# Optimization experiments

Hardware: AMD Instinct MI355X
Metric: run time of the kernel (lower is better)

Reference implementation:

```python
import jax, jax.numpy as jnp
import numpy as np

N, D, E, L = 50000, 64, 800000, 2


def _normalize(x):
    n = jnp.linalg.norm(x, axis=-1, keepdims=True)
    return x / jnp.maximum(n, 1e-12)


def _mobius_add(x, y, c):
    xy = jnp.sum(x * y, -1, keepdims=True)
    x2 = jnp.sum(x * x, -1, keepdims=True)
    y2 = jnp.sum(y * y, -1, keepdims=True)
    num = (1 + 2 * c * xy + c * y2) * x + (1 - c * x2) * y
    den = 1 + 2 * c * xy + (c ** 2) * x2 * y2
    return num / den


def _log_map(x, y, c):
    d = _mobius_add(-x, y, c)
    dn = jnp.maximum(jnp.linalg.norm(d, axis=-1, keepdims=True), 1e-10)
    return 2.0 / jnp.sqrt(c) * jnp.arctanh(jnp.sqrt(c) * dn) * d / dn


def _exp_map(x, v, c):
    vn = jnp.maximum(jnp.linalg.norm(v, axis=-1, keepdims=True), 1e-10)
    second = jnp.tanh(jnp.sqrt(c) * vn / 2.0) * v / (jnp.sqrt(c) * vn)
    return _mobius_add(x, second, c)


def _mean_agg(h, src, dst, n):
    # copy_u('h') then mean over incoming edges; empty neighborhoods -> 0 (DGL semantics)
    s = jax.ops.segment_sum(h[src], dst, num_segments=n)
    cnt = jax.ops.segment_sum(jnp.ones((src.shape[0],), h.dtype), dst, num_segments=n)
    return s / jnp.maximum(cnt, 1.0)[:, None]


def setup_inputs() -> dict:
    key = jax.random.key(0)
    ks = jax.random.split(key, 12)
    scale = 1.0 / np.sqrt(D)
    e_emb = jax.random.normal(ks[0], (N, D), jnp.float32)
    b_emb = jax.random.normal(ks[1], (N, D), jnp.float32) * (0.3 * scale)  # inside Poincare ball
    s_emb = jax.random.normal(ks[2], (N, D), jnp.float32)
    src = jax.random.randint(ks[3], (E,), 0, N, jnp.int32)
    dst = jax.random.randint(ks[4], (E,), 0, N, jnp.int32)
    We = jax.random.normal(ks[5], (L, D, D), jnp.float32) * scale
    Wb = jax.random.normal(ks[6], (L, D, D), jnp.float32) * scale
    Ws = jax.random.normal(ks[7], (L, D, D), jnp.float32) * scale
    be = jnp.zeros((L, D), jnp.float32)
    bb = jnp.zeros((L, D), jnp.float32)
    bs = jnp.zeros((L, D), jnp.float32)
    b_curvature = jnp.ones((1,), jnp.float32)
    s_curvature = jnp.ones((1,), jnp.float32)
    return {"e_emb": e_emb, "b_emb": b_emb, "s_emb": s_emb,
            "We": We, "be": be, "Wb": Wb, "bb": bb, "Ws": Ws, "bs": bs,
            "b_curvature": b_curvature, "s_curvature": s_curvature,
            "src": src, "dst": dst}


def reference(e_emb, b_emb, s_emb, We, be, Wb, bb, Ws, bs, b_curvature, s_curvature, src, dst):
    n = e_emb.shape[0]
    bc = b_curvature[0]
    sc = s_curvature[0]  # spherical path does not use curvature in the original forward math
    zero = jnp.zeros_like(b_emb)
    for l in range(We.shape[0]):
        # euclidean: linear -> mean aggregate -> LeakyReLU(0.2)
        h = e_emb @ We[l].T + be[l]
        e_emb = jax.nn.leaky_relu(_mean_agg(h, src, dst, n), 0.2)
        # hyperbolic: log map at origin -> linear -> mean aggregate -> exp map at origin
        tan = _log_map(zero, b_emb, bc)
        hb = tan @ Wb[l].T + bb[l]
        b_emb = _exp_map(zero, _mean_agg(hb, src, dst, n), bc)
        # spherical: normalize -> linear -> normalize -> mean aggregate -> normalize
        hs = _normalize(_normalize(s_emb) @ Ws[l].T + bs[l])
        s_emb = _normalize(_mean_agg(hs, src, dst, n))
    return (e_emb, b_emb, s_emb)
```

## Files before the change

kernel.cpp:

```cpp
#include <hip/hip_runtime.h>
#include <hip/hip_bf16.h>

#define DIM 64

typedef __attribute__((ext_vector_type(4)))  float f32x4;
typedef __attribute__((ext_vector_type(2)))  float f32x2;
typedef __attribute__((ext_vector_type(8)))  short short8;
typedef __attribute__((ext_vector_type(4)))  unsigned short u16x4;
typedef __attribute__((ext_vector_type(2)))  unsigned int u32x2;

static __device__ __forceinline__ float wave_sum64(float v) {
    v += __shfl_xor(v, 1, 64);
    v += __shfl_xor(v, 2, 64);
    v += __shfl_xor(v, 4, 64);
    v += __shfl_xor(v, 8, 64);
    v += __shfl_xor(v, 16, 64);
    v += __shfl_xor(v, 32, 64);
    return v;
}

static __device__ __forceinline__ float b2f(unsigned short u) {
    return __uint_as_float(((unsigned int)u) << 16);
}
static __device__ __forceinline__ unsigned short f2b(float f) {
    unsigned int u = __float_as_uint(f);
    unsigned int rounded = u + 0x7fff + ((u >> 16) & 1);
    return (unsigned short)(rounded >> 16);
}
static __device__ __forceinline__ float b2f_lo(unsigned int u) {
    return __uint_as_float(u << 16);
}
static __device__ __forceinline__ float b2f_hi(unsigned int u) {
    return __uint_as_float(u & 0xffff0000u);
}

#define PCHUNK 8192
#define BCAP 4096

__global__ __launch_bounds__(256) void k_wbhist(
        const float* __restrict__ We, const float* __restrict__ Wb,
        const float* __restrict__ Ws, unsigned short* __restrict__ wcvt,
        int L, int blocksW, unsigned short* __restrict__ hb_zero_row,
        const int* __restrict__ dst, int* __restrict__ bcnt, int E) {
    __shared__ int hist[1024];
    int bid = blockIdx.x;
    if (bid < blocksW) {
        int i = bid * 256 + threadIdx.x;
        int total = L * 3 * 4096;
        if (i >= total) return;
        int pos  = i & 4095;
        int lm   = i >> 12;
        int mode = lm % 3;
        int l    = lm / 3;
        const float* W = (mode == 0) ? We : (mode == 1) ? Wb : Ws;
        float v = W[(size_t)l * 4096 + pos];
        unsigned short hi = f2b(v);
        unsigned short lo = f2b(v - b2f(hi));
        wcvt[((size_t)lm * 2 + 0) * 4096 + pos] = hi;
        wcvt[((size_t)lm * 2 + 1) * 4096 + pos] = lo;
        return;
    }
    if (bid == blocksW) {
        if (threadIdx.x < 192) hb_zero_row[threadIdx.x] = 0;
        return;
    }
    int chunk = bid - blocksW - 1;
    int base = chunk * PCHUNK;
    int cnt = E - base; if (cnt > PCHUNK) cnt = PCHUNK;
    int t = threadIdx.x;
    for (int i = t; i < 1024; i += 256) hist[i] = 0;
    __syncthreads();
    for (int k = t; k < cnt; k += 256) {
        int b = dst[base + k] >> 6;
        atomicAdd(&hist[b], 1);
    }
    __syncthreads();
    for (int b = t; b < 1024; b += 256) {
        int h = hist[b];
        if (h > 0) atomicAdd(&bcnt[b], h);
    }
}

__global__ __launch_bounds__(1024) void k_bscan(const int* __restrict__ bcnt,
                                                int* __restrict__ bbase,
                                                int* __restrict__ bcur,
                                                int* __restrict__ row_start,
                                                int n, int E) {
    __shared__ int buf[1024];
    int t = threadIdx.x;
    int v = bcnt[t];
    buf[t] = v;
    __syncthreads();
    for (int off = 1; off < 1024; off <<= 1) {
        int x = (t >= off) ? buf[t - off] : 0;
        __syncthreads();
        buf[t] += x;
        __syncthreads();
    }
    int excl = buf[t] - v;
    bbase[t] = excl;
    bcur[t]  = excl;
    if (t == 1023) {
        bbase[1024] = buf[1023];
        row_start[n] = E;
    }
}

__global__ __launch_bounds__(256) void k_part(const int* __restrict__ src,
                                              const int* __restrict__ dst,
                                              int* __restrict__ bcur,
                                              unsigned int* __restrict__ ebuf,
                                              int E) {
    __shared__ int hist[1024];
    __shared__ int aux[256];
    __shared__ int delta[1024];
    __shared__ unsigned int stage[PCHUNK];

    int t = threadIdx.x;
    int base = blockIdx.x * PCHUNK;
    int cnt = E - base; if (cnt > PCHUNK) cnt = PCHUNK;

#pragma unroll
    for (int i = t; i < 1024; i += 256) hist[i] = 0;
    __syncthreads();

    for (int k = t; k < cnt; k += 256) {
        int b = dst[base + k] >> 6;
        atomicAdd(&hist[b], 1);
    }
    __syncthreads();

    int i4 = 4 * t;
    int a0 = hist[i4], a1 = hist[i4 + 1], a2 = hist[i4 + 2], a3 = hist[i4 + 3];
    int s = a0 + a1 + a2 + a3;
    aux[t] = s;
    __syncthreads();
    for (int off = 1; off < 256; off <<= 1) {
        int x = (t >= off) ? aux[t - off] : 0;
        __syncthreads();
        aux[t] += x;
        __syncthreads();
    }
    int excl = aux[t] - s;
    hist[i4]     = excl;
    hist[i4 + 1] = excl + a0;
    hist[i4 + 2] = excl + a0 + a1;
    hist[i4 + 3] = excl + a0 + a1 + a2;
    __syncthreads();

    int total = aux[255];
    for (int b = t; b < 1024; b += 256) {
        int st = hist[b];
        int nx = (b + 1 < 1024) ? hist[b + 1] : total;
        int cb = nx - st;
        if (cb > 0) {
            int gb = atomicAdd(&bcur[b], cb);
            delta[b] = gb - st;
        }
    }
    __syncthreads();

    for (int k = t; k < cnt; k += 256) {
        unsigned int d = (unsigned int)dst[base + k];
        unsigned int sv = (unsigned int)src[base + k];
        int b = (int)(d >> 6);
        int pos = atomicAdd(&hist[b], 1);
        stage[pos] = (d << 16) | sv;
    }
    __syncthreads();

    for (int p = t; p < cnt; p += 256) {
        unsigned int v = stage[p];
        int b = (int)(v >> 22);
        ebuf[delta[b] + p] = v;
    }
}

__global__ __launch_bounds__(256) void k_bfill2(const unsigned int* __restrict__ ebuf,
                                                const int* __restrict__ bbase,
                                                int* __restrict__ row_start,
                                                int* __restrict__ csr_src,
                                                int n) {
    __shared__ int cnt64[64];
    __shared__ int lcur[64];
    __shared__ unsigned int evals[BCAP];
    __shared__ int lcsr[BCAP];
    int b = blockIdx.x;
    int t = threadIdx.x;
    int nodeLo = b * 64;
    int gLo = bbase[b];
    int gHi = bbase[b + 1];
    int cntB = gHi - gLo;

    if (t < 64) cnt64[t] = 0;
    __syncthreads();

    if (cntB <= BCAP) {
        for (int p = t; p < cntB; p += 256) {
            unsigned int v = ebuf[gLo + p];
            evals[p] = v;
            atomicAdd(&cnt64[(int)(v >> 16) - nodeLo], 1);
        }
        __syncthreads();
        int v0 = (t < 64) ? cnt64[t] : 0;
        for (int off = 1; off < 64; off <<= 1) {
            int x = (t < 64 && t >= off) ? cnt64[t - off] : 0;
            __syncthreads();
            if (t < 64) cnt64[t] += x;
            __syncthreads();
        }
        if (t < 64) {
            int pref = cnt64[t] - v0;
            lcur[t] = pref;
            int node = nodeLo + t;
            if (node < n) row_start[node] = gLo + pref;
        }
        __syncthreads();
        for (int p = t; p < cntB; p += 256) {
            unsigned int v = evals[p];
            int li = (int)(v >> 16) - nodeLo;
            int slot = atomicAdd(&lcur[li], 1);
            lcsr[slot] = (int)(v & 0xFFFFu);
        }
        __syncthreads();
        for (int p = t; p < cntB; p += 256) csr_src[gLo + p] = lcsr[p];
    } else {
        for (int p = t; p < cntB; p += 256) {
            unsigned int v = ebuf[gLo + p];
            atomicAdd(&cnt64[(int)(v >> 16) - nodeLo], 1);
        }
        __syncthreads();
        int v0 = (t < 64) ? cnt64[t] : 0;
        for (int off = 1; off < 64; off <<= 1) {
            int x = (t < 64 && t >= off) ? cnt64[t - off] : 0;
            __syncthreads();
            if (t < 64) cnt64[t] += x;
            __syncthreads();
        }
        if (t < 64) {
            int pref = cnt64[t] - v0;
            lcur[t] = pref;
            int node = nodeLo + t;
            if (node < n) row_start[node] = gLo + pref;
        }
        __syncthreads();
        for (int p = t; p < cntB; p += 256) {
            unsigned int v = ebuf[gLo + p];
            int li = (int)(v >> 16) - nodeLo;
            int slot = atomicAdd(&lcur[li], 1);
            csr_src[gLo + slot] = (int)(v & 0xFFFFu);
        }
    }
}

__global__ void k_hist(const int* __restrict__ dst, int* __restrict__ cnt, int E) {
    int e = blockIdx.x * blockDim.x + threadIdx.x;
    if (e < E) atomicAdd(&cnt[dst[e]], 1);
}
__global__ __launch_bounds__(1024) void k_scan1(const int* __restrict__ cnt,
                                                int* __restrict__ partial,
                                                int* __restrict__ blocksum, int n) {
    __shared__ int buf[1024];
    int t = threadIdx.x;
    int i = blockIdx.x * 1024 + t;
    int v = (i < n) ? cnt[i] : 0;
    buf[t] = v;
    __syncthreads();
    for (int off = 1; off < 1024; off <<= 1) {
        int x = (t >= off) ? buf[t - off] : 0;
        __syncthreads();
        buf[t] += x;
        __syncthreads();
    }
    if (i < n) partial[i] = buf[t];
    if (t == 1023) blocksum[blockIdx.x] = buf[1023];
}
__global__ __launch_bounds__(1024) void k_scan2(int* __restrict__ blocksum, int nb) {
    __shared__ int buf[1024];
    int t = threadIdx.x;
    buf[t] = (t < nb) ? blocksum[t] : 0;
    __syncthreads();
    for (int off = 1; off < 1024; off <<= 1) {
        int x = (t >= off) ? buf[t - off] : 0;
        __syncthreads();
        buf[t] += x;
        __syncthreads();
    }
    if (t < nb) blocksum[t] = buf[t];
}
__global__ void k_scan3(const int* __restrict__ partial, const int* __restrict__ blocksum,
                        const int* __restrict__ cnt,
                        int* __restrict__ row_start, int* __restrict__ cursor, int n) {
    int i = blockIdx.x * blockDim.x + threadIdx.x;
    if (i == 0) row_start[0] = 0;
    if (i < n) {
        int b = i >> 10;
        int add = (b > 0) ? blocksum[b - 1] : 0;
        int incl = partial[i] + add;
        row_start[i + 1] = incl;
        cursor[i] = incl - cnt[i];
    }
}
__global__ void k_fill(const int* __restrict__ src, const int* __restrict__ dst,
                       int* __restrict__ cursor, int* __restrict__ csr_src, int E) {
    int e = blockIdx.x * blockDim.x + threadIdx.x;
    if (e < E) {
        int p = atomicAdd(&cursor[dst[e]], 1);
        csr_src[p] = src[e];
    }
}
__global__ __launch_bounds__(256) void k_wconv_fb(
        const float* __restrict__ We, const float* __restrict__ Wb,
        const float* __restrict__ Ws, unsigned short* __restrict__ wcvt,
        int L, int blocksW, unsigned short* __restrict__ hb_zero_row) {
    if ((int)blockIdx.x >= blocksW) {
        if (threadIdx.x < 192) hb_zero_row[threadIdx.x] = 0;
        return;
    }
    int i = blockIdx.x * 256 + threadIdx.x;
    int total = L * 3 * 4096;
    if (i >= total) return;
    int pos  = i & 4095;
    int lm   = i >> 12;
    int mode = lm % 3;
    int l    = lm / 3;
    const float* W = (mode == 0) ? We : (mode == 1) ? Wb : Ws;
    float v = W[(size_t)l * 4096 + pos];
    unsigned short hi = f2b(v);
    unsigned short lo = f2b(v - b2f(hi));
    wcvt[((size_t)lm * 2 + 0) * 4096 + pos] = hi;
    wcvt[((size_t)lm * 2 + 1) * 4096 + pos] = lo;
}

__global__ __launch_bounds__(256) void k_phaseA_mfma(
        const float* __restrict__ Xe, const float* __restrict__ Xb, const float* __restrict__ Xs,
        const unsigned short* __restrict__ wcvt,
        const float* __restrict__ be, const float* __restrict__ bb, const float* __restrict__ bs,
        unsigned short* __restrict__ hb, const float* __restrict__ curv,
        int n, int ntiles, int wavesPerMode) {
    int gtid = blockIdx.x * blockDim.x + threadIdx.x;
    int gw   = gtid >> 6;
    int lane = gtid & 63;
    int mode = gw / wavesPerMode;
    if (mode >= 3) return;
    int w0   = gw - mode * wavesPerMode;

    int mrow  = lane & 15;
    int half  = lane >> 4;

    const float* X    = (mode == 0) ? Xe : (mode == 1) ? Xb : Xs;
    const float* bias = (mode == 0) ? be : (mode == 1) ? bb : bs;
    float sc = sqrtf(curv[0]);

    const unsigned short* whi = wcvt + ((size_t)mode * 2 + 0) * 4096;
    const unsigned short* wlo = wcvt + ((size_t)mode * 2 + 1) * 4096;
    short8 b_hi[4][2], b_lo[4][2];
#pragma unroll
    for (int t = 0; t < 4; ++t) {
        int wrow = 16 * t + mrow;
#pragma unroll
        for (int kc = 0; kc < 2; ++kc) {
            int off = wrow * DIM + 32 * kc + 8 * half;
            b_hi[t][kc] = *reinterpret_cast<const short8*>(whi + off);
            b_lo[t][kc] = *reinterpret_cast<const short8*>(wlo + off);
        }
    }
    float bl[4];
#pragma unroll
    for (int t = 0; t < 4; ++t) bl[t] = bias[16 * t + mrow];

    for (int tile = w0; tile < ntiles; tile += wavesPerMode) {
        int node0 = tile * 16;
        int row = node0 + mrow;
        int rowc = (row < n) ? row : (n - 1);
        const float* xp = X + (size_t)rowc * DIM + 8 * half;
        float xv[16];
        {
            const float4* p0 = reinterpret_cast<const float4*>(xp);
            const float4* p1 = reinterpret_cast<const float4*>(xp + 32);
            float4 a = p0[0], b = p0[1], c = p1[0], d = p1[1];
            xv[0]=a.x; xv[1]=a.y; xv[2]=a.z; xv[3]=a.w;
            xv[4]=b.x; xv[5]=b.y; xv[6]=b.z; xv[7]=b.w;
            xv[8]=c.x; xv[9]=c.y; xv[10]=c.z; xv[11]=c.w;
            xv[12]=d.x; xv[13]=d.y; xv[14]=d.z; xv[15]=d.w;
        }

        float scale = 1.0f;
        if (mode != 0) {
            float ss = 0.f;
#pragma unroll
            for (int i = 0; i < 16; ++i) ss = fmaf(xv[i], xv[i], ss);
            ss += __shfl_xor(ss, 16, 64);
            ss += __shfl_xor(ss, 32, 64);
            if (mode == 1) {
                float dn = fmaxf(sqrtf(ss), 1e-10f);
                scale = (2.0f / sc) * atanhf(sc * dn) / dn;
            } else {
                float dn = fmaxf(sqrtf(ss), 1e-12f);
                scale = 1.0f / dn;
            }
        }

        short8 a_hi0, a_hi1, a_lo0, a_lo1;
#pragma unroll
        for (int i = 0; i < 8; ++i) {
            float s0 = xv[i] * scale;
            unsigned short h0 = f2b(s0);
            a_hi0[i] = (short)h0;
            a_lo0[i] = (short)f2b(s0 - b2f(h0));
            float s1 = xv[8 + i] * scale;
            unsigned short h1 = f2b(s1);
            a_hi1[i] = (short)h1;
            a_lo1[i] = (short)f2b(s1 - b2f(h1));
        }

        f32x4 acc[4];
#pragma unroll
        for (int t = 0; t < 4; ++t) {
            f32x4 a = {0.f, 0.f, 0.f, 0.f};
            a = __builtin_amdgcn_mfma_f32_16x16x32_bf16(a_hi0, b_hi[t][0], a, 0, 0, 0);
            a = __builtin_amdgcn_mfma_f32_16x16x32_bf16(a_hi1, b_hi[t][1], a, 0, 0, 0);
            a = __builtin_amdgcn_mfma_f32_16x16x32_bf16(a_lo0, b_hi[t][0], a, 0, 0, 0);
            a = __builtin_amdgcn_mfma_f32_16x16x32_bf16(a_lo1, b_hi[t][1], a, 0, 0, 0);
            a = __builtin_amdgcn_mfma_f32_16x16x32_bf16(a_hi0, b_lo[t][0], a, 0, 0, 0);
            a = __builtin_amdgcn_mfma_f32_16x16x32_bf16(a_hi1, b_lo[t][1], a, 0, 0, 0);
            acc[t] = a;
        }

        float v[4][4];
#pragma unroll
        for (int t = 0; t < 4; ++t) {
#pragma unroll
            for (int r = 0; r < 4; ++r) v[t][r] = acc[t][r] + bl[t];
        }

        if (mode == 2) {
#pragma unroll
            for (int r = 0; r < 4; ++r) {
                float s = v[0][r]*v[0][r] + v[1][r]*v[1][r] + v[2][r]*v[2][r] + v[3][r]*v[3][r];
                s += __shfl_xor(s, 1, 64);
                s += __shfl_xor(s, 2, 64);
                s += __shfl_xor(s, 4, 64);
                s += __shfl_xor(s, 8, 64);
                float inv = 1.0f / fmaxf(sqrtf(s), 1e-12f);
#pragma unroll
                for (int t = 0; t < 4; ++t) v[t][r] *= inv;
            }
        }

#pragma unroll
        for (int r = 0; r < 4; ++r) {
            int orow = node0 + half * 4 + r;
            if (orow < n) {
                u16x4 pk;
                pk.x = f2b(v[0][r]); pk.y = f2b(v[1][r]);
                pk.z = f2b(v[2][r]); pk.w = f2b(v[3][r]);
                *reinterpret_cast<u16x4*>(hb + (size_t)orow * 192 + mode * 64 + 4 * mrow) = pk;
            }
        }
    }
}

#define GL(i, gname, vt) \
    "v_readlane_b32 %[st], %[idx], " #i "\n\t" \
    "s_mul_i32 %[st], %[st], 384\n\t" \
    "v_add_u32 %[" vt "], %[st], %[lo]\n\t" \
    "global_load_dwordx2 %[" gname "], %[" vt "], %[bs]\n\t"

#define ACC2(gi) { \
    f32x2 v01, v23; \
    v01.x = b2f_lo(gi.x); v01.y = b2f_hi(gi.x); \
    v23.x = b2f_lo(gi.y); v23.y = b2f_hi(gi.y); \
    asm volatile("v_pk_add_f32 %0, %1, %0" : "+v"(a01) : "v"(v01)); \
    asm volatile("v_pk_add_f32 %0, %1, %0" : "+v"(a23) : "v"(v23)); }

__global__ __launch_bounds__(256) void k_phaseB(const unsigned short* __restrict__ hb,
                                                const int* __restrict__ row_start,
                                                const int* __restrict__ csr_src,
                                                float* __restrict__ e_out,
                                                float* __restrict__ b_out,
                                                float* __restrict__ s_out,
                                                const float* __restrict__ curv,
                                                int n) {
    __shared__ float smem[4][192];
    int gtid = blockIdx.x * blockDim.x + threadIdx.x;
    int wid  = gtid >> 6;
    int lane = threadIdx.x & 63;
    int w    = threadIdx.x >> 6;
    if (wid >= n) return;

    int beg = row_start[wid];
    int end = row_start[wid + 1];

    const void* hbp = (const void*)hb;
    unsigned int lane_off = (unsigned int)lane * 8u;
    bool active = lane < 48;

    f32x2 a01 = {0.f, 0.f};
    f32x2 a23 = {0.f, 0.f};

    if (active) {
        int li0 = beg + (lane & 15);
        int lic0 = (li0 < end) ? li0 : (end - 1);
        unsigned int tv0 = (end > beg) ? (unsigned int)csr_src[lic0] : (unsigned int)n;
        unsigned int idxv = (li0 < end) ? tv0 : (unsigned int)n;

        for (int j = beg; j < end; j += 16) {
            u32x2 g0, g1, g2, g3, g4, g5, g6, g7;
            u32x2 g8, g9, g10, g11, g12, g13, g14, g15;
            unsigned int st, vt0, vt1;
            asm volatile(
                GL(0,  "g0",  "vt0") GL(1,  "g1",  "vt1")
                GL(2,  "g2",  "vt0") GL(3,  "g3",  "vt1")
                GL(4,  "g4",  "vt0") GL(5,  "g5",  "vt1")
                GL(6,  "g6",  "vt0") GL(7,  "g7",  "vt1")
                GL(8,  "g8",  "vt0") GL(9,  "g9",  "vt1")
                GL(10, "g10", "vt0") GL(11, "g11", "vt1")
                GL(12, "g12", "vt0") GL(13, "g13", "vt1")
                GL(14, "g14", "vt0") GL(15, "g15", "vt1")
                : [g0]"=&v"(g0),  [g1]"=&v"(g1),  [g2]"=&v"(g2),  [g3]"=&v"(g3),
                  [g4]"=&v"(g4),  [g5]"=&v"(g5),  [g6]"=&v"(g6),  [g7]"=&v"(g7),
                  [g8]"=&v"(g8),  [g9]"=&v"(g9),  [g10]"=&v"(g10),[g11]"=&v"(g11),
                  [g12]"=&v"(g12),[g13]"=&v"(g13),[g14]"=&v"(g14),[g15]"=&v"(g15),
                  [st]"=&s"(st), [vt0]"=&v"(vt0), [vt1]"=&v"(vt1)
                : [idx]"v"(idxv), [lo]"v"(lane_off), [bs]"s"(hbp)
                : "memory");

            int jn = j + 16;
            unsigned int idx_next = idxv;
            if (jn < end) {
                int li = jn + (lane & 15);
                int lic = (li < end) ? li : (end - 1);
                unsigned int tv = (unsigned int)csr_src[lic];
                idx_next = (li < end) ? tv : (unsigned int)n;
            }

            asm volatile("s_waitcnt vmcnt(0)" ::: "memory");
            __builtin_amdgcn_sched_barrier(0);

            ACC2(g0)  ACC2(g1)  ACC2(g2)  ACC2(g3)
            ACC2(g4)  ACC2(g5)  ACC2(g6)  ACC2(g7)
            ACC2(g8)  ACC2(g9)  ACC2(g10) ACC2(g11)
            ACC2(g12) ACC2(g13) ACC2(g14) ACC2(g15)

            idxv = idx_next;
        }
        smem[w][4 * lane + 0] = a01.x;
        smem[w][4 * lane + 1] = a01.y;
        smem[w][4 * lane + 2] = a23.x;
        smem[w][4 * lane + 3] = a23.y;
    }
    asm volatile("s_waitcnt lgkmcnt(0)" ::: "memory");

    int c = 4 * (lane & 15) + (lane >> 4);
    float fe = smem[w][c];
    float fb = smem[w][64 + c];
    float fs = smem[w][128 + c];

    int cnt = end - beg;
    float inv = 1.0f / (float)(cnt > 0 ? cnt : 1);
    fe *= inv; fb *= inv; fs *= inv;

    e_out[(size_t)wid * DIM + lane] = (fe >= 0.f) ? fe : 0.2f * fe;

    float cc = curv[0];
    float sc = sqrtf(cc);
    float vn = fmaxf(sqrtf(wave_sum64(fb * fb)), 1e-10f);
    float scale = tanhf(sc * vn * 0.5f) / (sc * vn);
    b_out[(size_t)wid * DIM + lane] = fb * scale;

    float nr = fmaxf(sqrtf(wave_sum64(fs * fs)), 1e-12f);
    s_out[(size_t)wid * DIM + lane] = fs / nr;
}

extern "C" void kernel_launch(void* const* d_in, const int* in_sizes, int n_in,
                              void* d_out, int out_size, void* d_ws, size_t ws_size,
                              hipStream_t stream) {
    const float* e0   = (const float*)d_in[0];
    const float* b0   = (const float*)d_in[1];
    const float* s0   = (const float*)d_in[2];
    const float* We   = (const float*)d_in[3];
    const float* be   = (const float*)d_in[4];
    const float* Wb   = (const float*)d_in[5];
    const float* bb   = (const float*)d_in[6];
    const float* Ws   = (const float*)d_in[7];
    const float* bs   = (const float*)d_in[8];
    const float* bcurv= (const float*)d_in[9];
    const int*   src  = (const int*)d_in[11];
    const int*   dst  = (const int*)d_in[12];

    const int N = in_sizes[0] / DIM;
    const int E = in_sizes[11];
    const int L = in_sizes[3] / (DIM * DIM);

    const int Npad = (N + 1023) & ~1023;
    int* cnt       = (int*)d_ws;
    int* row_start = cnt + Npad;
    int* cursor    = row_start + Npad + 64;
    int* blocksum  = cursor + Npad;
    int* bcur      = blocksum + 1024;
    int* bcnt      = bcur + 1024;
    int* bbase     = bcnt + 1024;
    int* csr_src   = bbase + 1032;
    unsigned int* ebuf = (unsigned int*)(csr_src + ((E + 63) & ~63));
    unsigned short* hb   = (unsigned short*)(ebuf + ((E + 63) & ~63));
    unsigned short* wcvt = hb + (size_t)(N + 1) * 192;

    float* out_e = (float*)d_out;
    float* out_b = out_e + (size_t)N * DIM;
    float* out_s = out_b + (size_t)N * DIM;

    const int ntiles = (N + 15) / 16;
    const int wavesPerMode = 1024;
    const int grdA = (3 * wavesPerMode) / 4;
    const int grdE = (E + 255) / 256;
    const int grdB = (N * DIM + 255) / 256;
    const int wtot = L * 3 * 4096;
    const int grdW = (wtot + 255) / 256;
    const int NB2  = (N + 63) / 64;
    const int nchunk = (E + PCHUNK - 1) / PCHUNK;

    if (N <= 65536) {
        hipMemsetAsync(bcnt, 0, 1024 * sizeof(int), stream);
        k_wbhist<<<grdW + 1 + nchunk, 256, 0, stream>>>(
            We, Wb, Ws, wcvt, L, grdW, hb + (size_t)N * 192, dst, bcnt, E);
        k_bscan<<<1, 1024, 0, stream>>>(bcnt, bbase, bcur, row_start, N, E);
        k_part<<<nchunk, 256, 0, stream>>>(src, dst, bcur, ebuf, E);
        k_bfill2<<<NB2, 256, 0, stream>>>(ebuf, bbase, row_start, csr_src, N);
    } else {
        hipMemsetAsync(cnt, 0, (size_t)N * sizeof(int), stream);
        k_wconv_fb<<<grdW + 1, 256, 0, stream>>>(We, Wb, Ws, wcvt, L, grdW,
                                                 hb + (size_t)N * 192);
        k_hist<<<grdE, 256, 0, stream>>>(dst, cnt, E);
        int nb = (N + 1023) / 1024;
        k_scan1<<<nb, 1024, 0, stream>>>(cnt, cursor, blocksum, N);
        k_scan2<<<1, 1024, 0, stream>>>(blocksum, nb);
        k_scan3<<<(N + 255) / 256, 256, 0, stream>>>(cursor, blocksum, cnt,
                                                     row_start, cursor, N);
        k_fill<<<grdE, 256, 0, stream>>>(src, dst, cursor, csr_src, E);
    }

    for (int l = 0; l < L; ++l) {
        const float* Xe = (l == 0) ? e0 : out_e;
        const float* Xb = (l == 0) ? b0 : out_b;
        const float* Xs = (l == 0) ? s0 : out_s;

        k_phaseA_mfma<<<grdA, 256, 0, stream>>>(
            Xe, Xb, Xs,
            wcvt + (size_t)l * 3 * 2 * 4096,
            be + (size_t)l * DIM, bb + (size_t)l * DIM, bs + (size_t)l * DIM,
            hb, bcurv, N, ntiles, wavesPerMode);

        k_phaseB<<<grdB, 256, 0, stream>>>(hb, row_start, csr_src,
                                           out_e, out_b, out_s, bcurv, N);
    }
}
```

Measured before the change: 202.8 us.

## Co-launch layer-0 transform with edge partitioning in one merged kernel

The layer-0 per-node linear transform (phase A) no longer runs as its own launch. Its blocks are appended to the edge-partition kernel's grid, so the dense MFMA work runs alongside the scatter-based partitioning. This removes one launch and lets the compute-heavy and atomic/memory-heavy work overlap. Workspace buffers are also now placed with 256-byte alignment. The merged kernel reserves partition shared memory even for the phase-A blocks, which may lower their occupancy.

```diff
diff --git a/kernel.cpp b/kernel.cpp
--- a/kernel.cpp
+++ b/kernel.cpp
@@ -106,11 +106,158 @@
     }
 }
 
-__global__ __launch_bounds__(256) void k_part(const int* __restrict__ src,
-                                              const int* __restrict__ dst,
-                                              int* __restrict__ bcur,
-                                              unsigned int* __restrict__ ebuf,
-                                              int E) {
+static __device__ __forceinline__ void phaseA_body(
+        int gw, int lane,
+        const float* __restrict__ Xe, const float* __restrict__ Xb, const float* __restrict__ Xs,
+        const unsigned short* __restrict__ wcvt,
+        const float* __restrict__ be, const float* __restrict__ bb, const float* __restrict__ bs,
+        unsigned short* __restrict__ hb, const float* __restrict__ curv,
+        int n, int ntiles, int wavesPerMode) {
+    int mode = gw / wavesPerMode;
+    if (mode >= 3) return;
+    int w0   = gw - mode * wavesPerMode;
+
+    int mrow  = lane & 15;
+    int half  = lane >> 4;
+
+    const float* X    = (mode == 0) ? Xe : (mode == 1) ? Xb : Xs;
+    const float* bias = (mode == 0) ? be : (mode == 1) ? bb : bs;
+    float sc = sqrtf(curv[0]);
+
+    const unsigned short* whi = wcvt + ((size_t)mode * 2 + 0) * 4096;
+    const unsigned short* wlo = wcvt + ((size_t)mode * 2 + 1) * 4096;
+    short8 b_hi[4][2], b_lo[4][2];
+#pragma unroll
+    for (int t = 0; t < 4; ++t) {
+        int wrow = 16 * t + mrow;
+#pragma unroll
+        for (int kc = 0; kc < 2; ++kc) {
+            int off = wrow * DIM + 32 * kc + 8 * half;
+            b_hi[t][kc] = *reinterpret_cast<const short8*>(whi + off);
+            b_lo[t][kc] = *reinterpret_cast<const short8*>(wlo + off);
+        }
+    }
+    float bl[4];
+#pragma unroll
+    for (int t = 0; t < 4; ++t) bl[t] = bias[16 * t + mrow];
+
+    for (int tile = w0; tile < ntiles; tile += wavesPerMode) {
+        int node0 = tile * 16;
+        int row = node0 + mrow;
+        int rowc = (row < n) ? row : (n - 1);
+        const float* xp = X + (size_t)rowc * DIM + 8 * half;
+        float xv[16];
+        {
+            const float4* p0 = reinterpret_cast<const float4*>(xp);
+            const float4* p1 = reinterpret_cast<const float4*>(xp + 32);
+            float4 a = p0[0], b = p0[1], c = p1[0], d = p1[1];
+            xv[0]=a.x; xv[1]=a.y; xv[2]=a.z; xv[3]=a.w;
+            xv[4]=b.x; xv[5]=b.y; xv[6]=b.z; xv[7]=b.w;
+            xv[8]=c.x; xv[9]=c.y; xv[10]=c.z; xv[11]=c.w;
+            xv[12]=d.x; xv[13]=d.y; xv[14]=d.z; xv[15]=d.w;
+        }
+
+        float scale = 1.0f;
+        if (mode != 0) {
+            float ss = 0.f;
+#pragma unroll
+            for (int i = 0; i < 16; ++i) ss = fmaf(xv[i], xv[i], ss);
+            ss += __shfl_xor(ss, 16, 64);
+            ss += __shfl_xor(ss, 32, 64);
+            if (mode == 1) {
+                float dn = fmaxf(sqrtf(ss), 1e-10f);
+                scale = (2.0f / sc) * atanhf(sc * dn) / dn;
+            } else {
+                float dn = fmaxf(sqrtf(ss), 1e-12f);
+                scale = 1.0f / dn;
+            }
+        }
+
+        short8 a_hi0, a_hi1, a_lo0, a_lo1;
+#pragma unroll
+        for (int i = 0; i < 8; ++i) {
+            float s0 = xv[i] * scale;
+            unsigned short h0 = f2b(s0);
+            a_hi0[i] = (short)h0;
+            a_lo0[i] = (short)f2b(s0 - b2f(h0));
+            float s1 = xv[8 + i] * scale;
+            unsigned short h1 = f2b(s1);
+            a_hi1[i] = (short)h1;
+            a_lo1[i] = (short)f2b(s1 - b2f(h1));
+        }
+
+        f32x4 acc[4];
+#pragma unroll
+        for (int t = 0; t < 4; ++t) {
+            f32x4 a = {0.f, 0.f, 0.f, 0.f};
+            a = __builtin_amdgcn_mfma_f32_16x16x32_bf16(a_hi0, b_hi[t][0], a, 0, 0, 0);
+            a = __builtin_amdgcn_mfma_f32_16x16x32_bf16(a_hi1, b_hi[t][1], a, 0, 0, 0);
+            a = __builtin_amdgcn_mfma_f32_16x16x32_bf16(a_lo0, b_hi[t][0], a, 0, 0, 0);
+            a = __builtin_amdgcn_mfma_f32_16x16x32_bf16(a_lo1, b_hi[t][1], a, 0, 0, 0);
+            a = __builtin_amdgcn_mfma_f32_16x16x32_bf16(a_hi0, b_lo[t][0], a, 0, 0, 0);
+            a = __builtin_amdgcn_mfma_f32_16x16x32_bf16(a_hi1, b_lo[t][1], a, 0, 0, 0);
+            acc[t] = a;
+        }
+
+        float v[4][4];
+#pragma unroll
+        for (int t = 0; t < 4; ++t) {
+#pragma unroll
+            for (int r = 0; r < 4; ++r) v[t][r] = acc[t][r] + bl[t];
+        }
+
+        if (mode == 2) {
+#pragma unroll
+            for (int r = 0; r < 4; ++r) {
+                float s = v[0][r]*v[0][r] + v[1][r]*v[1][r] + v[2][r]*v[2][r] + v[3][r]*v[3][r];
+                s += __shfl_xor(s, 1, 64);
+                s += __shfl_xor(s, 2, 64);
+                s += __shfl_xor(s, 4, 64);
+                s += __shfl_xor(s, 8, 64);
+                float inv = 1.0f / fmaxf(sqrtf(s), 1e-12f);
+#pragma unroll
+                for (int t = 0; t < 4; ++t) v[t][r] *= inv;
+            }
+        }
+
+#pragma unroll
+        for (int r = 0; r < 4; ++r) {
+            int orow = node0 + half * 4 + r;
+            if (orow < n) {
+                u16x4 pk;
+                pk.x = f2b(v[0][r]); pk.y = f2b(v[1][r]);
+                pk.z = f2b(v[2][r]); pk.w = f2b(v[3][r]);
+                *reinterpret_cast<u16x4*>(hb + (size_t)orow * 192 + mode * 64 + 4 * mrow) = pk;
+            }
+        }
+    }
+}
+
+__global__ __launch_bounds__(256) void k_phaseA_mfma(
+        const float* __restrict__ Xe, const float* __restrict__ Xb, const float* __restrict__ Xs,
+        const unsigned short* __restrict__ wcvt,
+        const float* __restrict__ be, const float* __restrict__ bb, const float* __restrict__ bs,
+        unsigned short* __restrict__ hb, const float* __restrict__ curv,
+        int n, int ntiles, int wavesPerMode) {
+    int gtid = blockIdx.x * blockDim.x + threadIdx.x;
+    phaseA_body(gtid >> 6, gtid & 63, Xe, Xb, Xs, wcvt, be, bb, bs, hb, curv,
+                n, ntiles, wavesPerMode);
+}
+
+__global__ __launch_bounds__(256) void k_partA0(
+        const int* __restrict__ src, const int* __restrict__ dst,
+        int* __restrict__ bcur, unsigned int* __restrict__ ebuf, int E, int blocksP,
+        const float* __restrict__ Xe, const float* __restrict__ Xb, const float* __restrict__ Xs,
+        const unsigned short* __restrict__ wcvt,
+        const float* __restrict__ be, const float* __restrict__ bb, const float* __restrict__ bs,
+        unsigned short* __restrict__ hb, const float* __restrict__ curv,
+        int n, int ntiles, int wavesPerMode) {
+    if ((int)blockIdx.x >= blocksP) {
+        int gtid = (blockIdx.x - blocksP) * 256 + threadIdx.x;
+        phaseA_body(gtid >> 6, gtid & 63, Xe, Xb, Xs, wcvt, be, bb, bs, hb, curv,
+                    n, ntiles, wavesPerMode);
+        return;
+    }
     __shared__ int hist[1024];
     __shared__ int aux[256];
     __shared__ int delta[1024];
@@ -330,135 +477,6 @@
     unsigned short lo = f2b(v - b2f(hi));
     wcvt[((size_t)lm * 2 + 0) * 4096 + pos] = hi;
     wcvt[((size_t)lm * 2 + 1) * 4096 + pos] = lo;
-}
-
-__global__ __launch_bounds__(256) void k_phaseA_mfma(
-        const float* __restrict__ Xe, const float* __restrict__ Xb, const float* __restrict__ Xs,
-        const unsigned short* __restrict__ wcvt,
-        const float* __restrict__ be, const float* __restrict__ bb, const float* __restrict__ bs,
-        unsigned short* __restrict__ hb, const float* __restrict__ curv,
-        int n, int ntiles, int wavesPerMode) {
-    int gtid = blockIdx.x * blockDim.x + threadIdx.x;
-    int gw   = gtid >> 6;
-    int lane = gtid & 63;
-    int mode = gw / wavesPerMode;
-    if (mode >= 3) return;
-    int w0   = gw - mode * wavesPerMode;
-
-    int mrow  = lane & 15;
-    int half  = lane >> 4;
-
-    const float* X    = (mode == 0) ? Xe : (mode == 1) ? Xb : Xs;
-    const float* bias = (mode == 0) ? be : (mode == 1) ? bb : bs;
-    float sc = sqrtf(curv[0]);
-
-    const unsigned short* whi = wcvt + ((size_t)mode * 2 + 0) * 4096;
-    const unsigned short* wlo = wcvt + ((size_t)mode * 2 + 1) * 4096;
-    short8 b_hi[4][2], b_lo[4][2];
-#pragma unroll
-    for (int t = 0; t < 4; ++t) {
-        int wrow = 16 * t + mrow;
-#pragma unroll
-        for (int kc = 0; kc < 2; ++kc) {
-            int off = wrow * DIM + 32 * kc + 8 * half;
-            b_hi[t][kc] = *reinterpret_cast<const short8*>(whi + off);
-            b_lo[t][kc] = *reinterpret_cast<const short8*>(wlo + off);
-        }
-    }
-    float bl[4];
-#pragma unroll
-    for (int t = 0; t < 4; ++t) bl[t] = bias[16 * t + mrow];
-
-    for (int tile = w0; tile < ntiles; tile += wavesPerMode) {
-        int node0 = tile * 16;
-        int row = node0 + mrow;
-        int rowc = (row < n) ? row : (n - 1);
-        const float* xp = X + (size_t)rowc * DIM + 8 * half;
-        float xv[16];
-        {
-            const float4* p0 = reinterpret_cast<const float4*>(xp);
-            const float4* p1 = reinterpret_cast<const float4*>(xp + 32);
-            float4 a = p0[0], b = p0[1], c = p1[0], d = p1[1];
-            xv[0]=a.x; xv[1]=a.y; xv[2]=a.z; xv[3]=a.w;
-            xv[4]=b.x; xv[5]=b.y; xv[6]=b.z; xv[7]=b.w;
-            xv[8]=c.x; xv[9]=c.y; xv[10]=c.z; xv[11]=c.w;
-            xv[12]=d.x; xv[13]=d.y; xv[14]=d.z; xv[15]=d.w;
-        }
-
-        float scale = 1.0f;
-        if (mode != 0) {
-            float ss = 0.f;
-#pragma unroll
-            for (int i = 0; i < 16; ++i) ss = fmaf(xv[i], xv[i], ss);
-            ss += __shfl_xor(ss, 16, 64);
-            ss += __shfl_xor(ss, 32, 64);
-            if (mode == 1) {
-                float dn = fmaxf(sqrtf(ss), 1e-10f);
-                scale = (2.0f / sc) * atanhf(sc * dn) / dn;
-            } else {
-                float dn = fmaxf(sqrtf(ss), 1e-12f);
-                scale = 1.0f / dn;
-            }
-        }
-
-        short8 a_hi0, a_hi1, a_lo0, a_lo1;
-#pragma unroll
-        for (int i = 0; i < 8; ++i) {
-            float s0 = xv[i] * scale;
-            unsigned short h0 = f2b(s0);
-            a_hi0[i] = (short)h0;
-            a_lo0[i] = (short)f2b(s0 - b2f(h0));
-            float s1 = xv[8 + i] * scale;
-            unsigned short h1 = f2b(s1);
-            a_hi1[i] = (short)h1;
-            a_lo1[i] = (short)f2b(s1 - b2f(h1));
-        }
-
-        f32x4 acc[4];
-#pragma unroll
-        for (int t = 0; t < 4; ++t) {
-            f32x4 a = {0.f, 0.f, 0.f, 0.f};
-            a = __builtin_amdgcn_mfma_f32_16x16x32_bf16(a_hi0, b_hi[t][0], a, 0, 0, 0);
-            a = __builtin_amdgcn_mfma_f32_16x16x32_bf16(a_hi1, b_hi[t][1], a, 0, 0, 0);
-            a = __builtin_amdgcn_mfma_f32_16x16x32_bf16(a_lo0, b_hi[t][0], a, 0, 0, 0);
-            a = __builtin_amdgcn_mfma_f32_16x16x32_bf16(a_lo1, b_hi[t][1], a, 0, 0, 0);
-            a = __builtin_amdgcn_mfma_f32_16x16x32_bf16(a_hi0, b_lo[t][0], a, 0, 0, 0);
-            a = __builtin_amdgcn_mfma_f32_16x16x32_bf16(a_hi1, b_lo[t][1], a, 0, 0, 0);
-            acc[t] = a;
-        }
-
-        float v[4][4];
-#pragma unroll
-        for (int t = 0; t < 4; ++t) {
-#pragma unroll
-            for (int r = 0; r < 4; ++r) v[t][r] = acc[t][r] + bl[t];
-        }
-
-        if (mode == 2) {
-#pragma unroll
-            for (int r = 0; r < 4; ++r) {
-                float s = v[0][r]*v[0][r] + v[1][r]*v[1][r] + v[2][r]*v[2][r] + v[3][r]*v[3][r];
-                s += __shfl_xor(s, 1, 64);
-                s += __shfl_xor(s, 2, 64);
-                s += __shfl_xor(s, 4, 64);
-                s += __shfl_xor(s, 8, 64);
-                float inv = 1.0f / fmaxf(sqrtf(s), 1e-12f);
-#pragma unroll
-                for (int t = 0; t < 4; ++t) v[t][r] *= inv;
-            }
-        }
-
-#pragma unroll
-        for (int r = 0; r < 4; ++r) {
-            int orow = node0 + half * 4 + r;
-            if (orow < n) {
-                u16x4 pk;
-                pk.x = f2b(v[0][r]); pk.y = f2b(v[1][r]);
-                pk.z = f2b(v[2][r]); pk.w = f2b(v[3][r]);
-                *reinterpret_cast<u16x4*>(hb + (size_t)orow * 192 + mode * 64 + 4 * mrow) = pk;
-            }
-        }
-    }
 }
 
 #define GL(i, gname, vt) \
@@ -594,17 +612,25 @@
     const int L = in_sizes[3] / (DIM * DIM);
 
     const int Npad = (N + 1023) & ~1023;
-    int* cnt       = (int*)d_ws;
-    int* row_start = cnt + Npad;
-    int* cursor    = row_start + Npad + 64;
-    int* blocksum  = cursor + Npad;
-    int* bcur      = blocksum + 1024;
-    int* bcnt      = bcur + 1024;
-    int* bbase     = bcnt + 1024;
-    int* csr_src   = bbase + 1032;
-    unsigned int* ebuf = (unsigned int*)(csr_src + ((E + 63) & ~63));
-    unsigned short* hb   = (unsigned short*)(ebuf + ((E + 63) & ~63));
-    unsigned short* wcvt = hb + (size_t)(N + 1) * 192;
+    char* wsb = (char*)d_ws;
+    size_t off = 0;
+    auto alloc = [&](size_t bytes) -> void* {
+        off = (off + 255) & ~(size_t)255;
+        void* p = wsb + off;
+        off += bytes;
+        return p;
+    };
+    int* cnt       = (int*)alloc((size_t)Npad * 4);
+    int* row_start = (int*)alloc((size_t)(Npad + 64) * 4);
+    int* cursor    = (int*)alloc((size_t)Npad * 4);
+    int* blocksum  = (int*)alloc(1024 * 4);
+    int* bcur      = (int*)alloc(1024 * 4);
+    int* bcnt      = (int*)alloc(1024 * 4);
+    int* bbase     = (int*)alloc(1032 * 4);
+    int* csr_src   = (int*)alloc((size_t)E * 4);
+    unsigned int* ebuf = (unsigned int*)alloc((size_t)E * 4);
+    unsigned short* hb = (unsigned short*)alloc((size_t)(N + 1) * 192 * 2);
+    unsigned short* wcvt = (unsigned short*)alloc((size_t)L * 3 * 2 * 4096 * 2);
 
     float* out_e = (float*)d_out;
     float* out_b = out_e + (size_t)N * DIM;
@@ -625,8 +651,22 @@
         k_wbhist<<<grdW + 1 + nchunk, 256, 0, stream>>>(
             We, Wb, Ws, wcvt, L, grdW, hb + (size_t)N * 192, dst, bcnt, E);
         k_bscan<<<1, 1024, 0, stream>>>(bcnt, bbase, bcur, row_start, N, E);
-        k_part<<<nchunk, 256, 0, stream>>>(src, dst, bcur, ebuf, E);
+        k_partA0<<<nchunk + grdA, 256, 0, stream>>>(
+            src, dst, bcur, ebuf, E, nchunk,
+            e0, b0, s0, wcvt, be, bb, bs, hb, bcurv, N, ntiles, wavesPerMode);
         k_bfill2<<<NB2, 256, 0, stream>>>(ebuf, bbase, row_start, csr_src, N);
+
+        k_phaseB<<<grdB, 256, 0, stream>>>(hb, row_start, csr_src,
+                                           out_e, out_b, out_s, bcurv, N);
+        for (int l = 1; l < L; ++l) {
+            k_phaseA_mfma<<<grdA, 256, 0, stream>>>(
+                out_e, out_b, out_s,
+                wcvt + (size_t)l * 3 * 2 * 4096,
+                be + (size_t)l * DIM, bb + (size_t)l * DIM, bs + (size_t)l * DIM,
+                hb, bcurv, N, ntiles, wavesPerMode);
+            k_phaseB<<<grdB, 256, 0, stream>>>(hb, row_start, csr_src,
+                                               out_e, out_b, out_s, bcurv, N);
+        }
     } else {
         hipMemsetAsync(cnt, 0, (size_t)N * sizeof(int), stream);
         k_wconv_fb<<<grdW + 1, 256, 0, stream>>>(We, Wb, Ws, wcvt, L, grdW,
@@ -638,20 +678,17 @@
         k_scan3<<<(N + 255) / 256, 256, 0, stream>>>(cursor, blocksum, cnt,
                                                      row_start, cursor, N);
         k_fill<<<grdE, 256, 0, stream>>>(src, dst, cursor, csr_src, E);
-    }
-
-    for (int l = 0; l < L; ++l) {
-        const float* Xe = (l == 0) ? e0 : out_e;
-        const float* Xb = (l == 0) ? b0 : out_b;
-        const float* Xs = (l == 0) ? s0 : out_s;
-
-        k_phaseA_mfma<<<grdA, 256, 0, stream>>>(
-            Xe, Xb, Xs,
-            wcvt + (size_t)l * 3 * 2 * 4096,
-            be + (size_t)l * DIM, bb + (size_t)l * DIM, bs + (size_t)l * DIM,
-            hb, bcurv, N, ntiles, wavesPerMode);
-
-        k_phaseB<<<grdB, 256, 0, stream>>>(hb, row_start, csr_src,
-                                           out_e, out_b, out_s, bcurv, N);
-    }
-}
+        for (int l = 0; l < L; ++l) {
+            const float* Xe = (l == 0) ? e0 : out_e;
+            const float* Xb = (l == 0) ? b0 : out_b;
+            const float* Xs = (l == 0) ? s0 : out_s;
+            k_phaseA_mfma<<<grdA, 256, 0, stream>>>(
+                Xe, Xb, Xs,
+                wcvt + (size_t)l * 3 * 2 * 4096,
+                be + (size_t)l * DIM, bb + (size_t)l * DIM, bs + (size_t)l * DIM,
+                hb, bcurv, N, ntiles, wavesPerMode);
+            k_phaseB<<<grdB, 256, 0, stream>>>(hb, row_start, csr_src,
+                                               out_e, out_b, out_s, bcurv, N);
+        }
+    }
+}
```

New measurement: 170.8 us. 15.7% less time.
